# Kernel optimization log

Hardware: AMD Instinct MI355X
Metric: run time of the kernel (lower is better)

Reference implementation:

```python
import jax, jax.numpy as jnp
import numpy as np

NEG_SLOPE = 0.2
BN_EPS = 1e-5


def _gatv2(x, src, dst, Wl, Wr, att, b, N, concat):
    # x: [N, Cin]; src/dst: [E] (self-loops already appended)
    H, F = att.shape
    xl = (x @ Wl).reshape(N, H, F)  # source transform
    xr = (x @ Wr).reshape(N, H, F)  # target transform
    s = jax.nn.leaky_relu(xl[src] + xr[dst], NEG_SLOPE)  # [E,H,F]
    e = jnp.einsum('ehf,hf->eh', s, att)                  # [E,H]
    m = jax.ops.segment_max(e, dst, num_segments=N)       # [N,H]
    ex = jnp.exp(e - m[dst])
    den = jax.ops.segment_sum(ex, dst, num_segments=N)
    alpha = ex / den[dst]                                 # [E,H] softmax over in-edges
    out = jax.ops.segment_sum(alpha[:, :, None] * xl[src], dst, num_segments=N)  # [N,H,F]
    out = out.reshape(N, H * F) if concat else out.mean(axis=1)
    return out + b


def _bn_eval(x, g, b, rm, rv):
    return (x - rm) * jax.lax.rsqrt(rv + BN_EPS) * g + b


def setup_inputs() -> dict:
    key = jax.random.key(0)
    ks = jax.random.split(key, 16)
    N, E, Cin, Fh, H, Cout = 50000, 800000, 128, 64, 4, 128
    Hm = H * Fh  # 256
    d = {
        'x': jax.random.normal(ks[0], (N, Cin), jnp.float32),
        'edge_index': jax.random.randint(ks[1], (2, E), 0, N, jnp.int64),
        'Wl1': jax.random.normal(ks[2], (Cin, Hm), jnp.float32) / np.sqrt(Cin),
        'Wr1': jax.random.normal(ks[3], (Cin, Hm), jnp.float32) / np.sqrt(Cin),
        'att1': jax.random.normal(ks[4], (H, Fh), jnp.float32) / np.sqrt(Fh),
        'b1': jnp.zeros((Hm,), jnp.float32),
        'bn1_g': jax.random.uniform(ks[5], (Hm,), jnp.float32, 0.5, 1.5),
        'bn1_b': 0.1 * jax.random.normal(ks[6], (Hm,), jnp.float32),
        'bn1_m': jnp.zeros((Hm,), jnp.float32),
        'bn1_v': jnp.ones((Hm,), jnp.float32),
        'Wl2': jax.random.normal(ks[7], (Hm, Hm), jnp.float32) / np.sqrt(Hm),
        'Wr2': jax.random.normal(ks[8], (Hm, Hm), jnp.float32) / np.sqrt(Hm),
        'att2': jax.random.normal(ks[9], (H, Fh), jnp.float32) / np.sqrt(Fh),
        'b2': jnp.zeros((Hm,), jnp.float32),
        'bn2_g': jax.random.uniform(ks[10], (Hm,), jnp.float32, 0.5, 1.5),
        'bn2_b': 0.1 * jax.random.normal(ks[11], (Hm,), jnp.float32),
        'bn2_m': jnp.zeros((Hm,), jnp.float32),
        'bn2_v': jnp.ones((Hm,), jnp.float32),
        'Wl3': jax.random.normal(ks[12], (Hm, Cout), jnp.float32) / np.sqrt(Hm),
        'Wr3': jax.random.normal(ks[13], (Hm, Cout), jnp.float32) / np.sqrt(Hm),
        'att3': jax.random.normal(ks[14], (1, Cout), jnp.float32) / np.sqrt(Cout),
        'b3': jnp.zeros((Cout,), jnp.float32),
    }
    return d


def reference(x, edge_index, Wl1, Wr1, att1, b1, bn1_g, bn1_b, bn1_m, bn1_v,
              Wl2, Wr2, att2, b2, bn2_g, bn2_b, bn2_m, bn2_v,
              Wl3, Wr3, att3, b3):
    N = x.shape[0]
    loop = jnp.arange(N, dtype=edge_index.dtype)
    src = jnp.concatenate([edge_index[0], loop])  # add self-loops (PyG default)
    dst = jnp.concatenate([edge_index[1], loop])
    h = _gatv2(x, src, dst, Wl1, Wr1, att1, b1, N, True)
    h = jax.nn.elu(_bn_eval(h, bn1_g, bn1_b, bn1_m, bn1_v))  # dropout=identity (eval)
    h = _gatv2(h, src, dst, Wl2, Wr2, att2, b2, N, True)
    h = jax.nn.elu(_bn_eval(h, bn2_g, bn2_b, bn2_m, bn2_v))
    return _gatv2(h, src, dst, Wl3, Wr3, att3, b3, N, False)
```

## Files before the change

kernel.cpp:

```cpp
#include <hip/hip_runtime.h>
#include <math.h>

#define NEG_SLOPE 0.2f
#define BN_EPS 1e-5f

typedef _Float16 f16x8 __attribute__((ext_vector_type(8)));
typedef float f32x4 __attribute__((ext_vector_type(4)));
typedef _Float16 h2 __attribute__((ext_vector_type(2)));

union U2 { uint2 u; h2 h[2]; };
union U1 { unsigned u; h2 h; };

__device__ __forceinline__ void async_copy16(const void* g, void* l) {
  __builtin_amdgcn_global_load_lds(
      (const __attribute__((address_space(1))) void*)g,
      (__attribute__((address_space(3))) void*)l, 16, 0, 0);
}

__device__ __forceinline__ h2 shfl_xor_h2(h2 v, int off) {
  U1 c; c.h = v;
  c.u = __shfl_xor(c.u, off, 64);
  return c.h;
}

__device__ __forceinline__ unsigned int pack2f(float a, float b) {
  union { unsigned int u; _Float16 h[2]; } c;
  c.h[0] = (_Float16)a; c.h[1] = (_Float16)b; return c.u;
}
__device__ __forceinline__ uint2 pack4f(float4 v) {
  union { uint2 u2; _Float16 h[4]; } c;
  c.h[0] = (_Float16)v.x; c.h[1] = (_Float16)v.y;
  c.h[2] = (_Float16)v.z; c.h[3] = (_Float16)v.w;
  return c.u2;
}

__global__ void k_zero_i32(int* __restrict__ p, int n) {
  int i = blockIdx.x * blockDim.x + threadIdx.x;
  if (i < n) p[i] = 0;
}

__global__ void k_f2h(const float* __restrict__ in, unsigned int* __restrict__ out, int n2) {
  int i = blockIdx.x * blockDim.x + threadIdx.x;
  if (i < n2) {
    float2 v = reinterpret_cast<const float2*>(in)[i];
    out[i] = pack2f(v.x, v.y);
  }
}

__global__ void k_prep_w(const float* __restrict__ Wl, const float* __restrict__ Wr,
                         int K, int Ch, _Float16* __restrict__ WT) {
  int i = blockIdx.x * blockDim.x + threadIdx.x;
  int total = 2 * Ch * K;
  if (i >= total) return;
  int c = i / K, k = i % K;
  float v = (c < Ch) ? Wl[(size_t)k * Ch + c] : Wr[(size_t)k * Ch + (c - Ch)];
  WT[i] = (_Float16)v;
}

__global__ void k_count(const int* __restrict__ ei, int E, int N, int* __restrict__ deg) {
  int e = blockIdx.x * blockDim.x + threadIdx.x;
  int T = E + N;
  if (e >= T) return;
  int d = (e < E) ? ei[E + e] : (e - E);
  atomicAdd(&deg[d], 1);
}

__global__ __launch_bounds__(256) void k_bsum(const int* __restrict__ deg, int N,
                                              int* __restrict__ bsum) {
  int t = threadIdx.x;
  int i = blockIdx.x * 256 + t;
  int v = (i < N) ? deg[i] : 0;
  #pragma unroll
  for (int off = 32; off > 0; off >>= 1) v += __shfl_xor(v, off, 64);
  __shared__ int ws[4];
  if ((t & 63) == 0) ws[t >> 6] = v;
  __syncthreads();
  if (t == 0) bsum[blockIdx.x] = ws[0] + ws[1] + ws[2] + ws[3];
}

__global__ __launch_bounds__(1024) void k_bscan(int* __restrict__ bsum, int nb, int N,
                                                int* __restrict__ offs) {
  int t = threadIdx.x;
  int lane = t & 63, w = t >> 6;
  int v = (t < nb) ? bsum[t] : 0;
  int val = v;
  #pragma unroll
  for (int off = 1; off < 64; off <<= 1) {
    int x = __shfl_up(val, off, 64);
    if (lane >= off) val += x;
  }
  __shared__ int ws[16];
  if (lane == 63) ws[w] = val;
  __syncthreads();
  if (w == 0) {
    int s = (lane < 16) ? ws[lane] : 0;
    #pragma unroll
    for (int off = 1; off < 16; off <<= 1) {
      int x = __shfl_up(s, off, 64);
      if (lane >= off) s += x;
    }
    if (lane < 16) ws[lane] = s;
  }
  __syncthreads();
  int excl = (w > 0 ? ws[w - 1] : 0) + val - v;
  if (t < nb) bsum[t] = excl;
  if (t == nb - 1) offs[N] = excl + v;
}

__global__ __launch_bounds__(256) void k_boffs(const int* __restrict__ deg, int N,
                                               const int* __restrict__ bpre,
                                               int* __restrict__ offs, int* __restrict__ cursor) {
  int t = threadIdx.x;
  int i = blockIdx.x * 256 + t;
  int lane = t & 63, w = t >> 6;
  int v = (i < N) ? deg[i] : 0;
  int val = v;
  #pragma unroll
  for (int off = 1; off < 64; off <<= 1) {
    int x = __shfl_up(val, off, 64);
    if (lane >= off) val += x;
  }
  __shared__ int ws[4];
  if (lane == 63) ws[w] = val;
  __syncthreads();
  int wo = 0;
  #pragma unroll
  for (int k = 0; k < 4; ++k) if (k < w) wo += ws[k];
  int excl = bpre[blockIdx.x] + wo + val - v;
  if (i < N) { offs[i] = excl; cursor[i] = excl; }
}

__global__ void k_scatter(const int* __restrict__ ei, int E, int N,
                          int* __restrict__ cursor, int* __restrict__ csr_src) {
  int e = blockIdx.x * blockDim.x + threadIdx.x;
  int T = E + N;
  if (e < 4) csr_src[T + e] = 0;
  if (e >= T) return;
  int s, d;
  if (e < E) { s = ei[e]; d = ei[E + e]; } else { s = d = e - E; }
  int pos = atomicAdd(&cursor[d], 1);
  csr_src[pos] = s;
}

__global__ __launch_bounds__(256) void k_hgemm(const _Float16* __restrict__ A,
                                               const _Float16* __restrict__ BT,
                                               _Float16* __restrict__ C,
                                               int M, int Ntot, int K) {
  __shared__ _Float16 As[2][128 * 64];
  __shared__ _Float16 Bs[2][128 * 64];
  const int t = threadIdx.x;
  const int lane = t & 63, w = t >> 6;
  const int wr = w >> 1, wc = w & 1;
  const int bm0 = blockIdx.x * 128, bn0 = blockIdx.y * 128;
  f32x4 acc[4][4] = {};
  const int nkt = K >> 6;

  auto stage = [&](int b, int kt) {
    #pragma unroll
    for (int i = 0; i < 4; ++i) {
      int q = (i * 4 + w) * 64 + lane;
      int row = q >> 3, sl = q & 7;
      int ssrc = sl ^ (row & 7);
      int ga = bm0 + row; if (ga >= M) ga = M - 1;
      async_copy16(&A[(size_t)ga * K + kt * 64 + ssrc * 8], &As[b][q * 8]);
      async_copy16(&BT[(size_t)(bn0 + row) * K + kt * 64 + ssrc * 8], &Bs[b][q * 8]);
    }
  };

  stage(0, 0);
  for (int kt = 0; kt < nkt; ++kt) {
    int cur = kt & 1;
    if (kt + 1 < nkt) {
      stage(cur ^ 1, kt + 1);
      asm volatile("s_waitcnt vmcnt(8)" ::: "memory");
    } else {
      asm volatile("s_waitcnt vmcnt(0)" ::: "memory");
    }
    __builtin_amdgcn_s_barrier();
    #pragma unroll
    for (int ks = 0; ks < 2; ++ks) {
      f16x8 a[4], b[4];
      const int sl = ks * 4 + (lane >> 4);
      #pragma unroll
      for (int mi = 0; mi < 4; ++mi) {
        int row = wr * 64 + mi * 16 + (lane & 15);
        a[mi] = *(const f16x8*)&As[cur][(row * 8 + (sl ^ (row & 7))) * 8];
      }
      #pragma unroll
      for (int ni = 0; ni < 4; ++ni) {
        int row = wc * 64 + ni * 16 + (lane & 15);
        b[ni] = *(const f16x8*)&Bs[cur][(row * 8 + (sl ^ (row & 7))) * 8];
      }
      #pragma unroll
      for (int mi = 0; mi < 4; ++mi)
        #pragma unroll
        for (int ni = 0; ni < 4; ++ni)
          acc[mi][ni] = __builtin_amdgcn_mfma_f32_16x16x32_f16(a[mi], b[ni], acc[mi][ni], 0, 0, 0);
    }
    __builtin_amdgcn_s_barrier();
  }
  const int r0 = (lane >> 4) * 4;
  const int cc = lane & 15;
  #pragma unroll
  for (int mi = 0; mi < 4; ++mi) {
    #pragma unroll
    for (int r = 0; r < 4; ++r) {
      int row = bm0 + wr * 64 + mi * 16 + r0 + r;
      if (row >= M) continue;
      #pragma unroll
      for (int ni = 0; ni < 4; ++ni) {
        int col = bn0 + wc * 64 + ni * 16 + cc;
        C[(size_t)row * Ntot + col] = (_Float16)acc[mi][ni][r];
      }
    }
  }
}

__global__ __launch_bounds__(128) void k_gat4(const _Float16* __restrict__ xlr,
                                              const float* __restrict__ att, const float* __restrict__ bias,
                                              const float* __restrict__ g, const float* __restrict__ bb,
                                              const float* __restrict__ rm, const float* __restrict__ rv,
                                              const int* __restrict__ offs, const int* __restrict__ csr,
                                              int N, _Float16* __restrict__ hout) {
  const int n = blockIdx.x * 2 + (threadIdx.x >> 6);
  if (n >= N) return;
  const int l4 = (threadIdx.x & 63);
  const uint2* xbase = (const uint2*)xlr + l4;
  U2 xru; xru.u = xbase[(size_t)n * 128 + 64];
  const h2 xr0 = xru.h[0], xr1 = xru.h[1];
  const float4 at = reinterpret_cast<const float4*>(att)[l4];
  const h2 at0 = {(_Float16)at.x, (_Float16)at.y};
  const h2 at1 = {(_Float16)at.z, (_Float16)at.w};
  const h2 k02 = {(_Float16)0.2f, (_Float16)0.2f};
  const int j0 = offs[n], j1 = offs[n + 1];

  float m = -INFINITY, l = 0.f;
  float4 acc = make_float4(0.f, 0.f, 0.f, 0.f);

  int j = j0;
  int s1 = csr[j0], s2 = csr[j0 + 1];
  uint2 u1 = xbase[(size_t)s1 * 128];
  uint2 u2 = xbase[(size_t)s2 * 128];

  for (; j + 1 < j1; j += 2) {
    int s1n = csr[j + 2], s2n = csr[j + 3];
    uint2 u1n = xbase[(size_t)s1n * 128];
    uint2 u2n = xbase[(size_t)s2n * 128];

    U2 c1, c2; c1.u = u1; c2.u = u2;
    h2 sA = c1.h[0] + xr0, sB = c1.h[1] + xr1;
    sA = __builtin_elementwise_max(sA, sA * k02);
    sB = __builtin_elementwise_max(sB, sB * k02);
    h2 dp1 = sA * at0 + sB * at1;
    h2 sC = c2.h[0] + xr0, sD = c2.h[1] + xr1;
    sC = __builtin_elementwise_max(sC, sC * k02);
    sD = __builtin_elementwise_max(sD, sD * k02);
    h2 dp2 = sC * at0 + sD * at1;

    h2 q = __builtin_shufflevector(dp1, dp2, 0, 2) + __builtin_shufflevector(dp1, dp2, 1, 3);
    #pragma unroll
    for (int off = 1; off < 16; off <<= 1) q += shfl_xor_h2(q, off);
    float e1 = (float)q[0], e2 = (float)q[1];

    float emax = fmaxf(e1, e2);
    if (__any(emax > m + 8.f)) {
      float mn = fmaxf(m, emax);
      float c0 = __expf(m - mn);
      l *= c0; acc.x *= c0; acc.y *= c0; acc.z *= c0; acc.w *= c0;
      m = mn;
    }
    float p1 = __expf(e1 - m), p2 = __expf(e2 - m);
    l += p1 + p2;
    acc.x += p1 * (float)c1.h[0][0] + p2 * (float)c2.h[0][0];
    acc.y += p1 * (float)c1.h[0][1] + p2 * (float)c2.h[0][1];
    acc.z += p1 * (float)c1.h[1][0] + p2 * (float)c2.h[1][0];
    acc.w += p1 * (float)c1.h[1][1] + p2 * (float)c2.h[1][1];
    u1 = u1n; u2 = u2n;
  }
  if (j < j1) {
    U2 c1; c1.u = u1;
    h2 sA = c1.h[0] + xr0, sB = c1.h[1] + xr1;
    sA = __builtin_elementwise_max(sA, sA * k02);
    sB = __builtin_elementwise_max(sB, sB * k02);
    h2 q = sA * at0 + sB * at1;
    #pragma unroll
    for (int off = 1; off < 16; off <<= 1) q += shfl_xor_h2(q, off);
    float e1 = (float)q[0] + (float)q[1];
    if (__any(e1 > m + 8.f)) {
      float mn = fmaxf(m, e1);
      float c0 = __expf(m - mn);
      l *= c0; acc.x *= c0; acc.y *= c0; acc.z *= c0; acc.w *= c0;
      m = mn;
    }
    float p1 = __expf(e1 - m);
    l += p1;
    acc.x += p1 * (float)c1.h[0][0];
    acc.y += p1 * (float)c1.h[0][1];
    acc.z += p1 * (float)c1.h[1][0];
    acc.w += p1 * (float)c1.h[1][1];
  }
  const int c0i = 4 * l4;
  const float4 b4  = reinterpret_cast<const float4*>(bias)[l4];
  const float4 rm4 = reinterpret_cast<const float4*>(rm)[l4];
  const float4 rv4 = reinterpret_cast<const float4*>(rv)[l4];
  const float4 g4  = reinterpret_cast<const float4*>(g)[l4];
  const float4 bb4 = reinterpret_cast<const float4*>(bb)[l4];
  (void)c0i;
  float inv = 1.f / l;
  float4 o;
  o.x = (acc.x * inv + b4.x - rm4.x) * rsqrtf(rv4.x + BN_EPS) * g4.x + bb4.x;
  o.y = (acc.y * inv + b4.y - rm4.y) * rsqrtf(rv4.y + BN_EPS) * g4.y + bb4.y;
  o.z = (acc.z * inv + b4.z - rm4.z) * rsqrtf(rv4.z + BN_EPS) * g4.z + bb4.z;
  o.w = (acc.w * inv + b4.w - rm4.w) * rsqrtf(rv4.w + BN_EPS) * g4.w + bb4.w;
  o.x = o.x > 0.f ? o.x : (__expf(o.x) - 1.f);
  o.y = o.y > 0.f ? o.y : (__expf(o.y) - 1.f);
  o.z = o.z > 0.f ? o.z : (__expf(o.z) - 1.f);
  o.w = o.w > 0.f ? o.w : (__expf(o.w) - 1.f);
  ((uint2*)hout)[(size_t)n * 64 + l4] = pack4f(o);
}

__global__ __launch_bounds__(128) void k_gat1(const _Float16* __restrict__ xlr,
                                              const float* __restrict__ att, const float* __restrict__ bias,
                                              const int* __restrict__ offs, const int* __restrict__ csr,
                                              int N, float* __restrict__ out) {
  const int n = blockIdx.x * 2 + (threadIdx.x >> 6);
  if (n >= N) return;
  const int l2 = (threadIdx.x & 63);
  const unsigned int* xbase = (const unsigned int*)xlr + l2;
  U1 xru; xru.u = xbase[(size_t)n * 128 + 64];
  const h2 xr0 = xru.h;
  const float2 a2 = reinterpret_cast<const float2*>(att)[l2];
  const h2 at0 = {(_Float16)a2.x, (_Float16)a2.y};
  const h2 k02 = {(_Float16)0.2f, (_Float16)0.2f};
  const int j0 = offs[n], j1 = offs[n + 1];

  float m = -INFINITY, l = 0.f, acc0 = 0.f, acc1 = 0.f;

  int j = j0;
  int s1 = csr[j0], s2 = csr[j0 + 1];
  unsigned int u1 = xbase[(size_t)s1 * 128];
  unsigned int u2 = xbase[(size_t)s2 * 128];

  for (; j + 1 < j1; j += 2) {
    int s1n = csr[j + 2], s2n = csr[j + 3];
    unsigned int u1n = xbase[(size_t)s1n * 128];
    unsigned int u2n = xbase[(size_t)s2n * 128];

    U1 c1, c2; c1.u = u1; c2.u = u2;
    h2 sA = c1.h + xr0;
    sA = __builtin_elementwise_max(sA, sA * k02);
    h2 dp1 = sA * at0;
    h2 sC = c2.h + xr0;
    sC = __builtin_elementwise_max(sC, sC * k02);
    h2 dp2 = sC * at0;

    h2 q = __builtin_shufflevector(dp1, dp2, 0, 2) + __builtin_shufflevector(dp1, dp2, 1, 3);
    #pragma unroll
    for (int off = 1; off < 64; off <<= 1) q += shfl_xor_h2(q, off);
    float e1 = (float)q[0], e2 = (float)q[1];

    float emax = fmaxf(e1, e2);
    if (__any(emax > m + 8.f)) {
      float mn = fmaxf(m, emax);
      float c0 = __expf(m - mn);
      l *= c0; acc0 *= c0; acc1 *= c0;
      m = mn;
    }
    float p1 = __expf(e1 - m), p2 = __expf(e2 - m);
    l += p1 + p2;
    acc0 += p1 * (float)c1.h[0] + p2 * (float)c2.h[0];
    acc1 += p1 * (float)c1.h[1] + p2 * (float)c2.h[1];
    u1 = u1n; u2 = u2n;
  }
  if (j < j1) {
    U1 c1; c1.u = u1;
    h2 sA = c1.h + xr0;
    sA = __builtin_elementwise_max(sA, sA * k02);
    h2 q = sA * at0;
    #pragma unroll
    for (int off = 1; off < 64; off <<= 1) q += shfl_xor_h2(q, off);
    float e1 = (float)q[0] + (float)q[1];
    if (__any(e1 > m + 8.f)) {
      float mn = fmaxf(m, e1);
      float c0 = __expf(m - mn);
      l *= c0; acc0 *= c0; acc1 *= c0;
      m = mn;
    }
    float p1 = __expf(e1 - m);
    l += p1;
    acc0 += p1 * (float)c1.h[0];
    acc1 += p1 * (float)c1.h[1];
  }
  float inv = 1.f / l;
  const float2 b2 = reinterpret_cast<const float2*>(bias)[l2];
  float2 o = make_float2(acc0 * inv + b2.x, acc1 * inv + b2.y);
  reinterpret_cast<float2*>(out)[(size_t)n * 64 + l2] = o;
}

extern "C" void kernel_launch(void* const* d_in, const int* in_sizes, int n_in,
                              void* d_out, int out_size, void* d_ws, size_t ws_size,
                              hipStream_t stream) {
  const float* x    = (const float*)d_in[0];
  const int*   ei   = (const int*)d_in[1];
  const float* Wl1  = (const float*)d_in[2];
  const float* Wr1  = (const float*)d_in[3];
  const float* att1 = (const float*)d_in[4];
  const float* b1   = (const float*)d_in[5];
  const float* bn1g = (const float*)d_in[6];
  const float* bn1b = (const float*)d_in[7];
  const float* bn1m = (const float*)d_in[8];
  const float* bn1v = (const float*)d_in[9];
  const float* Wl2  = (const float*)d_in[10];
  const float* Wr2  = (const float*)d_in[11];
  const float* att2 = (const float*)d_in[12];
  const float* b2   = (const float*)d_in[13];
  const float* bn2g = (const float*)d_in[14];
  const float* bn2b = (const float*)d_in[15];
  const float* bn2m = (const float*)d_in[16];
  const float* bn2v = (const float*)d_in[17];
  const float* Wl3  = (const float*)d_in[18];
  const float* Wr3  = (const float*)d_in[19];
  const float* att3 = (const float*)d_in[20];
  const float* b3   = (const float*)d_in[21];

  const int Hm   = in_sizes[5];
  const int Cout = in_sizes[21];
  const int Cin  = in_sizes[2] / Hm;
  const int N    = in_sizes[0] / Cin;
  const int E    = in_sizes[1] / 2;
  const int T    = E + N;

  _Float16* x16 = (_Float16*)d_ws;
  _Float16* h   = x16 + (size_t)N * Cin;
  _Float16* xlr = h + (size_t)N * Hm;
  _Float16* WT1 = xlr + (size_t)N * 2 * Hm;
  _Float16* WT2 = WT1 + (size_t)2 * Hm * Cin;
  _Float16* WT3 = WT2 + (size_t)2 * Hm * Hm;
  int* deg    = (int*)(WT3 + (size_t)2 * Cout * Hm);
  int* offs   = deg + N;
  int* cursor = offs + N + 1;
  int* csr    = cursor + N;
  int* bsum   = csr + T + 4;

  const int nb = (N + 255) / 256;

  k_zero_i32<<<(N + 255) / 256, 256, 0, stream>>>(deg, N);
  k_count<<<(T + 255) / 256, 256, 0, stream>>>(ei, E, N, deg);
  k_bsum<<<nb, 256, 0, stream>>>(deg, N, bsum);
  k_bscan<<<1, 1024, 0, stream>>>(bsum, nb, N, offs);
  k_boffs<<<nb, 256, 0, stream>>>(deg, N, bsum, offs, cursor);
  k_scatter<<<(T + 255) / 256, 256, 0, stream>>>(ei, E, N, cursor, csr);

  int n2 = N * Cin / 2;
  k_f2h<<<(n2 + 255) / 256, 256, 0, stream>>>(x, (unsigned int*)x16, n2);
  k_prep_w<<<(2 * Hm * Cin + 255) / 256, 256, 0, stream>>>(Wl1, Wr1, Cin, Hm, WT1);
  k_prep_w<<<(2 * Hm * Hm + 255) / 256, 256, 0, stream>>>(Wl2, Wr2, Hm, Hm, WT2);
  k_prep_w<<<(2 * Cout * Hm + 255) / 256, 256, 0, stream>>>(Wl3, Wr3, Hm, Cout, WT3);

  const int mb = (N + 127) / 128;
  const int gb = (N + 1) / 2;

  k_hgemm<<<dim3(mb, 2 * Hm / 128), 256, 0, stream>>>(x16, WT1, xlr, N, 2 * Hm, Cin);
  k_gat4<<<gb, 128, 0, stream>>>(xlr, att1, b1, bn1g, bn1b, bn1m, bn1v, offs, csr, N, h);

  k_hgemm<<<dim3(mb, 2 * Hm / 128), 256, 0, stream>>>(h, WT2, xlr, N, 2 * Hm, Hm);
  k_gat4<<<gb, 128, 0, stream>>>(xlr, att2, b2, bn2g, bn2b, bn2m, bn2v, offs, csr, N, h);

  k_hgemm<<<dim3(mb, 2 * Cout / 128), 256, 0, stream>>>(h, WT3, xlr, N, 2 * Cout, Hm);
  k_gat1<<<gb, 128, 0, stream>>>(xlr, att3, b3, offs, csr, N, (float*)d_out);
}
```

Measured before the change: 405.2 us.

## Process multiple edges per wavefront in GAT aggregation with wide loads

Restructures the GAT aggregation kernels so each wavefront handles several edges at once. In k_gat4 each 16-lane group loads 16 fp16 features of one source node with 128-bit loads; in k_gat1 each 8-lane group does the same. Partial softmax state is combined across groups with shuffles at the end. Attention scores use fdot2 and DPP reductions instead of many shuffle steps. Attention vectors and BN scale/shift are precomputed once in a small prep kernel, and blocks grow to 4 nodes. The aim is more memory-level parallelism and fewer instructions on the gather, at the cost of more registers and of idle lanes on the tail edges of each node, which are padded and masked.

```diff
diff --git a/kernel.cpp b/kernel.cpp
--- a/kernel.cpp
+++ b/kernel.cpp
@@ -8,8 +8,7 @@
 typedef float f32x4 __attribute__((ext_vector_type(4)));
 typedef _Float16 h2 __attribute__((ext_vector_type(2)));
 
-union U2 { uint2 u; h2 h[2]; };
-union U1 { unsigned u; h2 h; };
+union F8 { f16x8 v; h2 h[4]; _Float16 s[8]; uint4 u; };
 
 __device__ __forceinline__ void async_copy16(const void* g, void* l) {
   __builtin_amdgcn_global_load_lds(
@@ -17,21 +16,23 @@
       (__attribute__((address_space(3))) void*)l, 16, 0, 0);
 }
 
-__device__ __forceinline__ h2 shfl_xor_h2(h2 v, int off) {
-  U1 c; c.h = v;
-  c.u = __shfl_xor(c.u, off, 64);
-  return c.h;
-}
-
 __device__ __forceinline__ unsigned int pack2f(float a, float b) {
   union { unsigned int u; _Float16 h[2]; } c;
   c.h[0] = (_Float16)a; c.h[1] = (_Float16)b; return c.u;
 }
-__device__ __forceinline__ uint2 pack4f(float4 v) {
-  union { uint2 u2; _Float16 h[4]; } c;
-  c.h[0] = (_Float16)v.x; c.h[1] = (_Float16)v.y;
-  c.h[2] = (_Float16)v.z; c.h[3] = (_Float16)v.w;
-  return c.u2;
+
+__device__ __forceinline__ float fdot2f(h2 a, h2 b, float c) {
+#if __has_builtin(__builtin_amdgcn_fdot2)
+  return __builtin_amdgcn_fdot2(a, b, c, false);
+#else
+  return fmaf((float)a[0], (float)b[0], fmaf((float)a[1], (float)b[1], c));
+#endif
+}
+
+template <int CTRL>
+__device__ __forceinline__ float dpp_xadd(float x) {
+  int yi = __builtin_amdgcn_mov_dpp(__builtin_bit_cast(int, x), CTRL, 0xF, 0xF, true);
+  return x + __builtin_bit_cast(float, yi);
 }
 
 __global__ void k_zero_i32(int* __restrict__ p, int n) {
@@ -57,6 +58,25 @@
   WT[i] = (_Float16)v;
 }
 
+__global__ __launch_bounds__(256) void k_prep_misc(
+    const float* __restrict__ att1, const float* __restrict__ att2, const float* __restrict__ att3,
+    const float* __restrict__ b1, const float* __restrict__ g1, const float* __restrict__ bb1,
+    const float* __restrict__ m1, const float* __restrict__ v1,
+    const float* __restrict__ b2, const float* __restrict__ g2, const float* __restrict__ bb2,
+    const float* __restrict__ m2, const float* __restrict__ v2,
+    _Float16* __restrict__ a16_1, _Float16* __restrict__ a16_2, _Float16* __restrict__ a16_3,
+    float* __restrict__ sc1, float* __restrict__ sh1,
+    float* __restrict__ sc2, float* __restrict__ sh2) {
+  int c = threadIdx.x;
+  a16_1[c] = (_Float16)att1[c];
+  a16_2[c] = (_Float16)att2[c];
+  if (c < 128) a16_3[c] = (_Float16)att3[c];
+  float s = g1[c] * rsqrtf(v1[c] + BN_EPS);
+  sc1[c] = s; sh1[c] = (b1[c] - m1[c]) * s + bb1[c];
+  s = g2[c] * rsqrtf(v2[c] + BN_EPS);
+  sc2[c] = s; sh2[c] = (b2[c] - m2[c]) * s + bb2[c];
+}
+
 __global__ void k_count(const int* __restrict__ ei, int E, int N, int* __restrict__ deg) {
   int e = blockIdx.x * blockDim.x + threadIdx.x;
   int T = E + N;
@@ -134,7 +154,7 @@
                           int* __restrict__ cursor, int* __restrict__ csr_src) {
   int e = blockIdx.x * blockDim.x + threadIdx.x;
   int T = E + N;
-  if (e < 4) csr_src[T + e] = 0;
+  if (e < 32) csr_src[T + e] = 0;
   if (e >= T) return;
   int s, d;
   if (e < E) { s = ei[e]; d = ei[E + e]; } else { s = d = e - E; }
@@ -216,185 +236,199 @@
   }
 }
 
-__global__ __launch_bounds__(128) void k_gat4(const _Float16* __restrict__ xlr,
-                                              const float* __restrict__ att, const float* __restrict__ bias,
-                                              const float* __restrict__ g, const float* __restrict__ bb,
-                                              const float* __restrict__ rm, const float* __restrict__ rv,
-                                              const int* __restrict__ offs, const int* __restrict__ csr,
-                                              int N, _Float16* __restrict__ hout) {
-  const int n = blockIdx.x * 2 + (threadIdx.x >> 6);
+__global__ __launch_bounds__(256) void k_gat4(
+    const _Float16* __restrict__ xlr,
+    const _Float16* __restrict__ att16,
+    const float* __restrict__ sc, const float* __restrict__ sh,
+    const int* __restrict__ offs, const int* __restrict__ csr,
+    int N, _Float16* __restrict__ hout) {
+  const int n = blockIdx.x * 4 + (threadIdx.x >> 6);
   if (n >= N) return;
-  const int l4 = (threadIdx.x & 63);
-  const uint2* xbase = (const uint2*)xlr + l4;
-  U2 xru; xru.u = xbase[(size_t)n * 128 + 64];
-  const h2 xr0 = xru.h[0], xr1 = xru.h[1];
-  const float4 at = reinterpret_cast<const float4*>(att)[l4];
-  const h2 at0 = {(_Float16)at.x, (_Float16)at.y};
-  const h2 at1 = {(_Float16)at.z, (_Float16)at.w};
-  const h2 k02 = {(_Float16)0.2f, (_Float16)0.2f};
+  const int lane = threadIdx.x & 63;
+  const int sub = lane & 15;
+  const int qi = lane >> 4;
+
+  const F8* xb = (const F8*)xlr;
+  const F8* ab = (const F8*)att16;
+
+  F8 at0 = ab[2 * sub], at1 = ab[2 * sub + 1];
+  F8 xr0 = xb[(size_t)n * 64 + 32 + 2 * sub];
+  F8 xr1 = xb[(size_t)n * 64 + 32 + 2 * sub + 1];
+  const h2 k02 = {(_Float16)NEG_SLOPE, (_Float16)NEG_SLOPE};
+
   const int j0 = offs[n], j1 = offs[n + 1];
 
   float m = -INFINITY, l = 0.f;
-  float4 acc = make_float4(0.f, 0.f, 0.f, 0.f);
-
-  int j = j0;
-  int s1 = csr[j0], s2 = csr[j0 + 1];
-  uint2 u1 = xbase[(size_t)s1 * 128];
-  uint2 u2 = xbase[(size_t)s2 * 128];
-
-  for (; j + 1 < j1; j += 2) {
-    int s1n = csr[j + 2], s2n = csr[j + 3];
-    uint2 u1n = xbase[(size_t)s1n * 128];
-    uint2 u2n = xbase[(size_t)s2n * 128];
-
-    U2 c1, c2; c1.u = u1; c2.u = u2;
-    h2 sA = c1.h[0] + xr0, sB = c1.h[1] + xr1;
-    sA = __builtin_elementwise_max(sA, sA * k02);
-    sB = __builtin_elementwise_max(sB, sB * k02);
-    h2 dp1 = sA * at0 + sB * at1;
-    h2 sC = c2.h[0] + xr0, sD = c2.h[1] + xr1;
-    sC = __builtin_elementwise_max(sC, sC * k02);
-    sD = __builtin_elementwise_max(sD, sD * k02);
-    h2 dp2 = sC * at0 + sD * at1;
-
-    h2 q = __builtin_shufflevector(dp1, dp2, 0, 2) + __builtin_shufflevector(dp1, dp2, 1, 3);
-    #pragma unroll
-    for (int off = 1; off < 16; off <<= 1) q += shfl_xor_h2(q, off);
-    float e1 = (float)q[0], e2 = (float)q[1];
-
-    float emax = fmaxf(e1, e2);
-    if (__any(emax > m + 8.f)) {
-      float mn = fmaxf(m, emax);
-      float c0 = __expf(m - mn);
-      l *= c0; acc.x *= c0; acc.y *= c0; acc.z *= c0; acc.w *= c0;
-      m = mn;
-    }
-    float p1 = __expf(e1 - m), p2 = __expf(e2 - m);
-    l += p1 + p2;
-    acc.x += p1 * (float)c1.h[0][0] + p2 * (float)c2.h[0][0];
-    acc.y += p1 * (float)c1.h[0][1] + p2 * (float)c2.h[0][1];
-    acc.z += p1 * (float)c1.h[1][0] + p2 * (float)c2.h[1][0];
-    acc.w += p1 * (float)c1.h[1][1] + p2 * (float)c2.h[1][1];
-    u1 = u1n; u2 = u2n;
-  }
-  if (j < j1) {
-    U2 c1; c1.u = u1;
-    h2 sA = c1.h[0] + xr0, sB = c1.h[1] + xr1;
-    sA = __builtin_elementwise_max(sA, sA * k02);
-    sB = __builtin_elementwise_max(sB, sB * k02);
-    h2 q = sA * at0 + sB * at1;
-    #pragma unroll
-    for (int off = 1; off < 16; off <<= 1) q += shfl_xor_h2(q, off);
-    float e1 = (float)q[0] + (float)q[1];
-    if (__any(e1 > m + 8.f)) {
-      float mn = fmaxf(m, e1);
-      float c0 = __expf(m - mn);
-      l *= c0; acc.x *= c0; acc.y *= c0; acc.z *= c0; acc.w *= c0;
-      m = mn;
-    }
-    float p1 = __expf(e1 - m);
-    l += p1;
-    acc.x += p1 * (float)c1.h[0][0];
-    acc.y += p1 * (float)c1.h[0][1];
-    acc.z += p1 * (float)c1.h[1][0];
-    acc.w += p1 * (float)c1.h[1][1];
-  }
-  const int c0i = 4 * l4;
-  const float4 b4  = reinterpret_cast<const float4*>(bias)[l4];
-  const float4 rm4 = reinterpret_cast<const float4*>(rm)[l4];
-  const float4 rv4 = reinterpret_cast<const float4*>(rv)[l4];
-  const float4 g4  = reinterpret_cast<const float4*>(g)[l4];
-  const float4 bb4 = reinterpret_cast<const float4*>(bb)[l4];
-  (void)c0i;
-  float inv = 1.f / l;
-  float4 o;
-  o.x = (acc.x * inv + b4.x - rm4.x) * rsqrtf(rv4.x + BN_EPS) * g4.x + bb4.x;
-  o.y = (acc.y * inv + b4.y - rm4.y) * rsqrtf(rv4.y + BN_EPS) * g4.y + bb4.y;
-  o.z = (acc.z * inv + b4.z - rm4.z) * rsqrtf(rv4.z + BN_EPS) * g4.z + bb4.z;
-  o.w = (acc.w * inv + b4.w - rm4.w) * rsqrtf(rv4.w + BN_EPS) * g4.w + bb4.w;
-  o.x = o.x > 0.f ? o.x : (__expf(o.x) - 1.f);
-  o.y = o.y > 0.f ? o.y : (__expf(o.y) - 1.f);
-  o.z = o.z > 0.f ? o.z : (__expf(o.z) - 1.f);
-  o.w = o.w > 0.f ? o.w : (__expf(o.w) - 1.f);
-  ((uint2*)hout)[(size_t)n * 64 + l4] = pack4f(o);
-}
-
-__global__ __launch_bounds__(128) void k_gat1(const _Float16* __restrict__ xlr,
-                                              const float* __restrict__ att, const float* __restrict__ bias,
-                                              const int* __restrict__ offs, const int* __restrict__ csr,
-                                              int N, float* __restrict__ out) {
-  const int n = blockIdx.x * 2 + (threadIdx.x >> 6);
+  float acc[16];
+  #pragma unroll
+  for (int i = 0; i < 16; ++i) acc[i] = 0.f;
+
+  int sA = csr[j0 + qi];
+  int sB = csr[j0 + 4 + qi];
+  F8 v0 = xb[(size_t)sA * 64 + 2 * sub];
+  F8 v1 = xb[(size_t)sA * 64 + 2 * sub + 1];
+
+  for (int j = j0; j < j1; ) {
+    F8 n0 = xb[(size_t)sB * 64 + 2 * sub];
+    F8 n1 = xb[(size_t)sB * 64 + 2 * sub + 1];
+    int sC = csr[j + 8 + qi];
+
+    float e = 0.f;
+    #pragma unroll
+    for (int r = 0; r < 4; ++r) {
+      h2 s0 = v0.h[r] + xr0.h[r];
+      s0 = __builtin_elementwise_max(s0, s0 * k02);
+      e = fdot2f(s0, at0.h[r], e);
+      h2 s1 = v1.h[r] + xr1.h[r];
+      s1 = __builtin_elementwise_max(s1, s1 * k02);
+      e = fdot2f(s1, at1.h[r], e);
+    }
+    e = dpp_xadd<0xB1>(e);
+    e = dpp_xadd<0x4E>(e);
+    if (j + qi >= j1) e = -1e30f;
+
+    if (__any(e > m + 8.f)) {
+      float mc = fmaxf(m, e);
+      mc = fmaxf(mc, __shfl_xor(mc, 16, 64));
+      mc = fmaxf(mc, __shfl_xor(mc, 32, 64));
+      float c0 = __expf(m - mc);
+      l *= c0;
+      #pragma unroll
+      for (int i = 0; i < 16; ++i) acc[i] *= c0;
+      m = mc;
+    }
+    float p = __expf(e - m);
+    l += p;
+    #pragma unroll
+    for (int i = 0; i < 8; ++i) acc[i] = fmaf(p, (float)v0.s[i], acc[i]);
+    #pragma unroll
+    for (int i = 0; i < 8; ++i) acc[8 + i] = fmaf(p, (float)v1.s[i], acc[8 + i]);
+    v0 = n0; v1 = n1; sB = sC; j += 4;
+  }
+  l += __shfl_xor(l, 16, 64);
+  l += __shfl_xor(l, 32, 64);
+  #pragma unroll
+  for (int i = 0; i < 16; ++i) {
+    acc[i] += __shfl_xor(acc[i], 16, 64);
+    acc[i] += __shfl_xor(acc[i], 32, 64);
+  }
+  if (qi == 0) {
+    float inv = 1.f / l;
+    const float4* sc4 = (const float4*)sc;
+    const float4* sh4 = (const float4*)sh;
+    float ov[16];
+    #pragma unroll
+    for (int k = 0; k < 4; ++k) {
+      float4 s4 = sc4[4 * sub + k], t4 = sh4[4 * sub + k];
+      ov[4 * k + 0] = acc[4 * k + 0] * inv * s4.x + t4.x;
+      ov[4 * k + 1] = acc[4 * k + 1] * inv * s4.y + t4.y;
+      ov[4 * k + 2] = acc[4 * k + 2] * inv * s4.z + t4.z;
+      ov[4 * k + 3] = acc[4 * k + 3] * inv * s4.w + t4.w;
+    }
+    #pragma unroll
+    for (int i = 0; i < 16; ++i) ov[i] = ov[i] > 0.f ? ov[i] : (__expf(ov[i]) - 1.f);
+    F8 o0, o1;
+    #pragma unroll
+    for (int i = 0; i < 8; ++i) { o0.s[i] = (_Float16)ov[i]; o1.s[i] = (_Float16)ov[8 + i]; }
+    F8* ob = (F8*)hout;
+    ob[(size_t)n * 32 + 2 * sub] = o0;
+    ob[(size_t)n * 32 + 2 * sub + 1] = o1;
+  }
+}
+
+__global__ __launch_bounds__(256) void k_gat1(
+    const _Float16* __restrict__ xlr,
+    const _Float16* __restrict__ att16,
+    const float* __restrict__ bias,
+    const int* __restrict__ offs, const int* __restrict__ csr,
+    int N, float* __restrict__ out) {
+  const int n = blockIdx.x * 4 + (threadIdx.x >> 6);
   if (n >= N) return;
-  const int l2 = (threadIdx.x & 63);
-  const unsigned int* xbase = (const unsigned int*)xlr + l2;
-  U1 xru; xru.u = xbase[(size_t)n * 128 + 64];
-  const h2 xr0 = xru.h;
-  const float2 a2 = reinterpret_cast<const float2*>(att)[l2];
-  const h2 at0 = {(_Float16)a2.x, (_Float16)a2.y};
-  const h2 k02 = {(_Float16)0.2f, (_Float16)0.2f};
+  const int lane = threadIdx.x & 63;
+  const int sub = lane & 7;
+  const int gi = lane >> 3;
+
+  const F8* xb = (const F8*)xlr;
+  const F8* ab = (const F8*)att16;
+  F8 at0 = ab[2 * sub], at1 = ab[2 * sub + 1];
+  F8 xr0 = xb[(size_t)n * 32 + 16 + 2 * sub];
+  F8 xr1 = xb[(size_t)n * 32 + 16 + 2 * sub + 1];
+  const h2 k02 = {(_Float16)NEG_SLOPE, (_Float16)NEG_SLOPE};
+
   const int j0 = offs[n], j1 = offs[n + 1];
-
-  float m = -INFINITY, l = 0.f, acc0 = 0.f, acc1 = 0.f;
-
-  int j = j0;
-  int s1 = csr[j0], s2 = csr[j0 + 1];
-  unsigned int u1 = xbase[(size_t)s1 * 128];
-  unsigned int u2 = xbase[(size_t)s2 * 128];
-
-  for (; j + 1 < j1; j += 2) {
-    int s1n = csr[j + 2], s2n = csr[j + 3];
-    unsigned int u1n = xbase[(size_t)s1n * 128];
-    unsigned int u2n = xbase[(size_t)s2n * 128];
-
-    U1 c1, c2; c1.u = u1; c2.u = u2;
-    h2 sA = c1.h + xr0;
-    sA = __builtin_elementwise_max(sA, sA * k02);
-    h2 dp1 = sA * at0;
-    h2 sC = c2.h + xr0;
-    sC = __builtin_elementwise_max(sC, sC * k02);
-    h2 dp2 = sC * at0;
-
-    h2 q = __builtin_shufflevector(dp1, dp2, 0, 2) + __builtin_shufflevector(dp1, dp2, 1, 3);
-    #pragma unroll
-    for (int off = 1; off < 64; off <<= 1) q += shfl_xor_h2(q, off);
-    float e1 = (float)q[0], e2 = (float)q[1];
-
-    float emax = fmaxf(e1, e2);
-    if (__any(emax > m + 8.f)) {
-      float mn = fmaxf(m, emax);
-      float c0 = __expf(m - mn);
-      l *= c0; acc0 *= c0; acc1 *= c0;
-      m = mn;
-    }
-    float p1 = __expf(e1 - m), p2 = __expf(e2 - m);
-    l += p1 + p2;
-    acc0 += p1 * (float)c1.h[0] + p2 * (float)c2.h[0];
-    acc1 += p1 * (float)c1.h[1] + p2 * (float)c2.h[1];
-    u1 = u1n; u2 = u2n;
-  }
-  if (j < j1) {
-    U1 c1; c1.u = u1;
-    h2 sA = c1.h + xr0;
-    sA = __builtin_elementwise_max(sA, sA * k02);
-    h2 q = sA * at0;
-    #pragma unroll
-    for (int off = 1; off < 64; off <<= 1) q += shfl_xor_h2(q, off);
-    float e1 = (float)q[0] + (float)q[1];
-    if (__any(e1 > m + 8.f)) {
-      float mn = fmaxf(m, e1);
-      float c0 = __expf(m - mn);
-      l *= c0; acc0 *= c0; acc1 *= c0;
-      m = mn;
-    }
-    float p1 = __expf(e1 - m);
-    l += p1;
-    acc0 += p1 * (float)c1.h[0];
-    acc1 += p1 * (float)c1.h[1];
-  }
-  float inv = 1.f / l;
-  const float2 b2 = reinterpret_cast<const float2*>(bias)[l2];
-  float2 o = make_float2(acc0 * inv + b2.x, acc1 * inv + b2.y);
-  reinterpret_cast<float2*>(out)[(size_t)n * 64 + l2] = o;
+  float m = -INFINITY, l = 0.f;
+  float acc[16];
+  #pragma unroll
+  for (int i = 0; i < 16; ++i) acc[i] = 0.f;
+
+  int sA = csr[j0 + gi];
+  int sB = csr[j0 + 8 + gi];
+  F8 v0 = xb[(size_t)sA * 32 + 2 * sub];
+  F8 v1 = xb[(size_t)sA * 32 + 2 * sub + 1];
+
+  for (int j = j0; j < j1; ) {
+    F8 n0 = xb[(size_t)sB * 32 + 2 * sub];
+    F8 n1 = xb[(size_t)sB * 32 + 2 * sub + 1];
+    int sC = csr[j + 16 + gi];
+
+    float e = 0.f;
+    #pragma unroll
+    for (int r = 0; r < 4; ++r) {
+      h2 s0 = v0.h[r] + xr0.h[r];
+      s0 = __builtin_elementwise_max(s0, s0 * k02);
+      e = fdot2f(s0, at0.h[r], e);
+      h2 s1 = v1.h[r] + xr1.h[r];
+      s1 = __builtin_elementwise_max(s1, s1 * k02);
+      e = fdot2f(s1, at1.h[r], e);
+    }
+    e = dpp_xadd<0xB1>(e);
+    e = dpp_xadd<0x4E>(e);
+    e += __shfl_xor(e, 4, 64);
+    if (j + gi >= j1) e = -1e30f;
+
+    if (__any(e > m + 8.f)) {
+      float mc = fmaxf(m, e);
+      mc = fmaxf(mc, __shfl_xor(mc, 8, 64));
+      mc = fmaxf(mc, __shfl_xor(mc, 16, 64));
+      mc = fmaxf(mc, __shfl_xor(mc, 32, 64));
+      float c0 = __expf(m - mc);
+      l *= c0;
+      #pragma unroll
+      for (int i = 0; i < 16; ++i) acc[i] *= c0;
+      m = mc;
+    }
+    float p = __expf(e - m);
+    l += p;
+    #pragma unroll
+    for (int i = 0; i < 8; ++i) acc[i] = fmaf(p, (float)v0.s[i], acc[i]);
+    #pragma unroll
+    for (int i = 0; i < 8; ++i) acc[8 + i] = fmaf(p, (float)v1.s[i], acc[8 + i]);
+    v0 = n0; v1 = n1; sB = sC; j += 8;
+  }
+  l += __shfl_xor(l, 8, 64);
+  l += __shfl_xor(l, 16, 64);
+  l += __shfl_xor(l, 32, 64);
+  #pragma unroll
+  for (int i = 0; i < 16; ++i) {
+    acc[i] += __shfl_xor(acc[i], 8, 64);
+    acc[i] += __shfl_xor(acc[i], 16, 64);
+    acc[i] += __shfl_xor(acc[i], 32, 64);
+  }
+  if (gi == 0) {
+    float inv = 1.f / l;
+    const float4* b4 = (const float4*)bias;
+    float4* ob = (float4*)out;
+    #pragma unroll
+    for (int k = 0; k < 4; ++k) {
+      float4 bb = b4[4 * sub + k];
+      float4 o;
+      o.x = acc[4 * k + 0] * inv + bb.x;
+      o.y = acc[4 * k + 1] * inv + bb.y;
+      o.z = acc[4 * k + 2] * inv + bb.z;
+      o.w = acc[4 * k + 3] * inv + bb.w;
+      ob[(size_t)n * 32 + 4 * sub + k] = o;
+    }
+  }
 }
 
 extern "C" void kernel_launch(void* const* d_in, const int* in_sizes, int n_in,
@@ -436,11 +470,18 @@
   _Float16* WT1 = xlr + (size_t)N * 2 * Hm;
   _Float16* WT2 = WT1 + (size_t)2 * Hm * Cin;
   _Float16* WT3 = WT2 + (size_t)2 * Hm * Hm;
-  int* deg    = (int*)(WT3 + (size_t)2 * Cout * Hm);
+  _Float16* a16_1 = WT3 + (size_t)2 * Cout * Hm;
+  _Float16* a16_2 = a16_1 + 256;
+  _Float16* a16_3 = a16_2 + 256;
+  float* sc1 = (float*)(a16_3 + 128);
+  float* sh1 = sc1 + 256;
+  float* sc2 = sh1 + 256;
+  float* sh2 = sc2 + 256;
+  int* deg    = (int*)(sh2 + 256);
   int* offs   = deg + N;
   int* cursor = offs + N + 1;
   int* csr    = cursor + N;
-  int* bsum   = csr + T + 4;
+  int* bsum   = csr + T + 32;
 
   const int nb = (N + 255) / 256;
 
@@ -456,16 +497,20 @@
   k_prep_w<<<(2 * Hm * Cin + 255) / 256, 256, 0, stream>>>(Wl1, Wr1, Cin, Hm, WT1);
   k_prep_w<<<(2 * Hm * Hm + 255) / 256, 256, 0, stream>>>(Wl2, Wr2, Hm, Hm, WT2);
   k_prep_w<<<(2 * Cout * Hm + 255) / 256, 256, 0, stream>>>(Wl3, Wr3, Hm, Cout, WT3);
+  k_prep_misc<<<1, 256, 0, stream>>>(att1, att2, att3,
+                                     b1, bn1g, bn1b, bn1m, bn1v,
+                                     b2, bn2g, bn2b, bn2m, bn2v,
+                                     a16_1, a16_2, a16_3, sc1, sh1, sc2, sh2);
 
   const int mb = (N + 127) / 128;
-  const int gb = (N + 1) / 2;
+  const int gb = (N + 3) / 4;
 
   k_hgemm<<<dim3(mb, 2 * Hm / 128), 256, 0, stream>>>(x16, WT1, xlr, N, 2 * Hm, Cin);
-  k_gat4<<<gb, 128, 0, stream>>>(xlr, att1, b1, bn1g, bn1b, bn1m, bn1v, offs, csr, N, h);
+  k_gat4<<<gb, 256, 0, stream>>>(xlr, a16_1, sc1, sh1, offs, csr, N, h);
 
   k_hgemm<<<dim3(mb, 2 * Hm / 128), 256, 0, stream>>>(h, WT2, xlr, N, 2 * Hm, Hm);
-  k_gat4<<<gb, 128, 0, stream>>>(xlr, att2, b2, bn2g, bn2b, bn2m, bn2v, offs, csr, N, h);
+  k_gat4<<<gb, 256, 0, stream>>>(xlr, a16_2, sc2, sh2, offs, csr, N, h);
 
   k_hgemm<<<dim3(mb, 2 * Cout / 128), 256, 0, stream>>>(h, WT3, xlr, N, 2 * Cout, Hm);
-  k_gat1<<<gb, 128, 0, stream>>>(xlr, att3, b3, offs, csr, N, (float*)d_out);
-}
+  k_gat1<<<gb, 256, 0, stream>>>(xlr, a16_3, b3, offs, csr, N, (float*)d_out);
+}
```

Measured after the change: 378.9 us. 1.07x faster.
